# Kernel tuning notes

Measured on AMD Instinct MI355X. Metric: run time of the kernel, lower is better.

Reference implementation:

```python
import jax, jax.numpy as jnp
import numpy as np

N_NODES = 10000
N_EDGES = 160000
C = 128          # hidden_channels
H = 8            # heads
G = 16           # groups
L_LAYERS = 5
NUM_FEAT = 14
DIM_OUT = 16
CH = C // H      # channels per head (16)


def setup_inputs() -> dict:
    key = jax.random.key(0)
    ks = jax.random.split(key, 12)
    inp = {
        "x": jax.random.normal(ks[0], (N_NODES, NUM_FEAT), dtype=jnp.float32),
        "edge_index": jax.random.randint(ks[1], (2, N_EDGES), 0, N_NODES, dtype=jnp.int64),
        "lin1_w": jax.random.normal(ks[2], (NUM_FEAT, C), dtype=jnp.float32) * 0.1,
        "lin1_b": jax.random.normal(ks[3], (C,), dtype=jnp.float32) * 0.1,
        "Wq": jax.random.normal(ks[4], (L_LAYERS, G, C // G, C // G), dtype=jnp.float32) * 0.1,
        "bq": jax.random.normal(ks[5], (L_LAYERS, C), dtype=jnp.float32) * 0.1,
        "Wk": jax.random.normal(ks[6], (L_LAYERS, G, C // G, C // G), dtype=jnp.float32) * 0.1,
        "bk": jax.random.normal(ks[7], (L_LAYERS, C), dtype=jnp.float32) * 0.1,
        "Wv": jax.random.normal(ks[8], (L_LAYERS, G, C // G, C // G), dtype=jnp.float32) * 0.1,
        "bv": jax.random.normal(ks[9], (L_LAYERS, C), dtype=jnp.float32) * 0.1,
        "lin2_w": jax.random.normal(ks[10], (C, DIM_OUT), dtype=jnp.float32) * 0.1,
        "lin2_b": jax.random.normal(ks[11], (DIM_OUT,), dtype=jnp.float32) * 0.1,
    }
    return inp


def _grouped_linear(z, W, b):
    # z: [..., C]; W: [G, C/G, C/G]; b: [C]  (PyG grouped Linear)
    lead = z.shape[:-1]
    zg = z.reshape(lead + (G, C // G))
    out = jnp.einsum('...gi,gio->...go', zg, W)
    return out.reshape(lead + (C,)) + b


def _dna_forward(x, edge_index, lin1_w, lin1_b, Wq, bq, Wk, bk, Wv, bv, lin2_w, lin2_b):
    n = x.shape[0]
    # gcn_norm with self-loops (edge_weight = 1)
    loops = jnp.arange(n, dtype=edge_index.dtype)
    row = jnp.concatenate([edge_index[0], loops])  # sources (x_j)
    col = jnp.concatenate([edge_index[1], loops])  # targets (x_i, aggregation)
    ew = jnp.ones(row.shape[0], dtype=x.dtype)
    deg = jax.ops.segment_sum(ew, col, num_segments=n)
    dis = jax.lax.rsqrt(deg)  # deg >= 1 due to self-loops
    norm = dis[row] * dis[col]  # [Et]

    h = jax.nn.relu(x @ lin1_w + lin1_b)  # [N, C]
    x_all = h[:, None, :]                  # [N, 1, C]

    scale = 1.0 / np.sqrt(CH).astype(np.float32)
    for l in range(L_LAYERS):
        q = _grouped_linear(x_all[col, -1], Wq[l], bq[l])   # [Et, C]
        k = _grouped_linear(x_all[row], Wk[l], bk[l])       # [Et, L, C]
        v = _grouped_linear(x_all[row], Wv[l], bv[l])       # [Et, L, C]
        Et, Lh = k.shape[0], k.shape[1]
        qh = q.reshape(Et, H, CH)
        kh = k.reshape(Et, Lh, H, CH)
        vh = v.reshape(Et, Lh, H, CH)
        score = jnp.einsum('ehc,elhc->ehl', qh, kh) * scale
        attn = jax.nn.softmax(score, axis=-1)
        out = jnp.einsum('ehl,elhc->ehc', attn, vh).reshape(Et, C)
        msg = norm[:, None] * out
        agg = jax.ops.segment_sum(msg, col, num_segments=n)  # [N, C]
        xl = jax.nn.relu(agg)
        x_all = jnp.concatenate([x_all, xl[:, None, :]], axis=1)

    return x_all[:, -1] @ lin2_w + lin2_b  # [N, dim]


def reference(x, edge_index, lin1_w, lin1_b, Wq, bq, Wk, bk, Wv, bv, lin2_w, lin2_b):
    return _dna_forward(x, edge_index, lin1_w, lin1_b, Wq, bq, Wk, bk, Wv, bv,
                        lin2_w, lin2_b)
```

## Files before the change

kernel.cpp:

```cpp
#include <hip/hip_runtime.h>

#define N_NODES 10000
#define N_EDGESN 160000
#define E_TOT   (N_EDGESN + N_NODES)
#define C 128
#define H 8
#define G 16
#define LLAYERS 5
#define NUM_FEAT 14
#define DIM_OUT 16
#define CH 16
#define CG 8
#define X16STRIDE (6*C)

typedef _Float16 half8 __attribute__((ext_vector_type(8)));
typedef _Float16 half2v __attribute__((ext_vector_type(2)));

__global__ __launch_bounds__(256) void k_lin1(const float* __restrict__ x,
                                              const float* __restrict__ w,
                                              const float* __restrict__ b,
                                              _Float16* __restrict__ x16,
                                              int* __restrict__ counts) {
    __shared__ float sw[NUM_FEAT * C];
    __shared__ float sb[C];
    int tid = threadIdx.x;
    int gid = blockIdx.x * 256 + tid;
    if (gid < N_NODES) counts[gid] = 0;
    for (int i = tid; i < NUM_FEAT * C; i += 256) sw[i] = w[i];
    if (tid < C) sb[tid] = b[tid];
    __syncthreads();
    int node = blockIdx.x * 2 + tid / C;
    int c = tid & (C - 1);
    if (node >= N_NODES) return;
    const float* xr = x + node * NUM_FEAT;
    float acc = sb[c];
#pragma unroll
    for (int f = 0; f < NUM_FEAT; f++) acc += xr[f] * sw[f * C + c];
    acc = fmaxf(acc, 0.0f);
    x16[(size_t)node * X16STRIDE + c] = (_Float16)acc;
}

__global__ void k_count(const int* __restrict__ col, int* __restrict__ counts) {
    int e = blockIdx.x * blockDim.x + threadIdx.x;
    if (e < N_EDGESN) atomicAdd(&counts[col[e]], 1);
}

__global__ __launch_bounds__(1024) void k_scan(const int* __restrict__ counts,
                                               int* __restrict__ offs, int* __restrict__ cursor,
                                               float* __restrict__ dis,
                                               int* __restrict__ bucket_cur) {
    __shared__ int part[1024];
    __shared__ int hist[256];
    const int CHK = (N_NODES + 1023) / 1024;
    int t = threadIdx.x;
    if (t < 256) hist[t] = 0;
    __syncthreads();
    int base = t * CHK;
    int loc[CHK];
    int sum = 0;
#pragma unroll
    for (int i = 0; i < CHK; i++) {
        int idx = base + i;
        int v = (idx < N_NODES) ? (counts[idx] + 1) : 0;
        loc[i] = sum;
        sum += v;
        if (idx < N_NODES) atomicAdd(&hist[min(v, 255)], 1);
    }
    part[t] = sum;
    __syncthreads();
    for (int off = 1; off < 1024; off <<= 1) {
        int v = (t >= off) ? part[t - off] : 0;
        __syncthreads();
        part[t] += v;
        __syncthreads();
    }
    int prev = (t > 0) ? part[t - 1] : 0;
#pragma unroll
    for (int i = 0; i < CHK; i++) {
        int idx = base + i;
        if (idx < N_NODES) {
            int o = prev + loc[i];
            offs[idx] = o;
            cursor[idx] = o;
            dis[idx] = rsqrtf((float)(counts[idx] + 1));
        }
    }
    if (t == 1023) offs[N_NODES] = part[1023];
    __syncthreads();
    if (t == 0) {
        int acc = 0;
        for (int d2 = 255; d2 >= 0; d2--) { int h = hist[d2]; hist[d2] = acc; acc += h; }
    }
    __syncthreads();
    if (t < 256) bucket_cur[t] = hist[t];
}

__global__ void k_scatter(const int* __restrict__ row, const int* __restrict__ col,
                          const float* __restrict__ dis, const int* __restrict__ counts,
                          int* __restrict__ cursor, int2* __restrict__ csr,
                          int* __restrict__ bucket_cur, int* __restrict__ perm) {
    int e = blockIdx.x * blockDim.x + threadIdx.x;
    if (e < N_NODES) {
        int deg = min(counts[e] + 1, 255);
        int pos = atomicAdd(&bucket_cur[deg], 1);
        perm[pos] = e;
    }
    if (e >= E_TOT) return;
    int r = (e < N_EDGESN) ? row[e] : (e - N_EDGESN);
    int c = (e < N_EDGESN) ? col[e] : (e - N_EDGESN);
    int pos = atomicAdd(&cursor[c], 1);
    int2 pay;
    pay.x = r;
    pay.y = __float_as_int(dis[r]);
    csr[pos] = pay;
}

template <int NL>
__global__ __launch_bounds__(256) void k_attn_fly(const int* __restrict__ offs,
                                                  const int2* __restrict__ csr,
                                                  const float* __restrict__ dis,
                                                  const int* __restrict__ perm,
                                                  const float* __restrict__ Wq, const float* __restrict__ bq,
                                                  const float* __restrict__ Wk, const float* __restrict__ bk,
                                                  const float* __restrict__ Wv, const float* __restrict__ bv,
                                                  _Float16* __restrict__ x16) {
    const int l = NL - 1;
    int w = threadIdx.x >> 6;
    int lane = threadIdx.x & 63;
    int d = perm[blockIdx.x * 4 + w];
    int g = lane >> 2;
    int j4 = lane & 3;
    int c0 = 2 * lane;
    int o0 = 2 * j4;

    float y8[8];
    float z = 0.f;
    if constexpr (NL > 1) {
        half8 hq = *(const half8*)(x16 + (size_t)d * X16STRIDE + l * C + 8 * g);
        float xdv[8];
#pragma unroll
        for (int i = 0; i < 8; i++) xdv[i] = (float)hq[i];
        const float* bqg = bq + l * C + 8 * g;
        float4 qa = *(const float4*)bqg;
        float4 qb = *(const float4*)(bqg + 4);
        const float* wq = Wq + l * (G * CG * CG) + g * (CG * CG);
#pragma unroll
        for (int i = 0; i < 8; i++) {
            float4 ra = *(const float4*)(wq + i * CG);
            float4 rb = *(const float4*)(wq + i * CG + 4);
            qa.x += xdv[i] * ra.x; qa.y += xdv[i] * ra.y;
            qa.z += xdv[i] * ra.z; qa.w += xdv[i] * ra.w;
            qb.x += xdv[i] * rb.x; qb.y += xdv[i] * rb.y;
            qb.z += xdv[i] * rb.z; qb.w += xdv[i] * rb.w;
        }
        const float* wk = Wk + l * (G * CG * CG) + g * (CG * CG);
#pragma unroll
        for (int j = 0; j < 8; j++) {
            float4 ra = *(const float4*)(wk + j * CG);
            float4 rb = *(const float4*)(wk + j * CG + 4);
            y8[j] = qa.x * ra.x + qa.y * ra.y + qa.z * ra.z + qa.w * ra.w
                  + qb.x * rb.x + qb.y * rb.y + qb.z * rb.z + qb.w * rb.w;
        }
        const float* bkg = bk + l * C + 8 * g;
        float4 ba = *(const float4*)bkg;
        float4 bb = *(const float4*)(bkg + 4);
        z = qa.x * ba.x + qa.y * ba.y + qa.z * ba.z + qa.w * ba.w
          + qb.x * bb.x + qb.y * bb.y + qb.z * bb.z + qb.w * bb.w;
    }

    const float disd = dis[d];
    const int p0 = offs[d], p1 = offs[d + 1];
    const float scale = 0.25f;
    float xacc[8] = {0.f, 0.f, 0.f, 0.f, 0.f, 0.f, 0.f, 0.f};
    float nsum = 0.f;

    if constexpr (NL == 1) {
        for (int p = p0 + j4; p < p1; p += 4) {
            int2 pay = csr[p];
            float nrm = disd * __int_as_float(pay.y);
            half8 hv = *(const half8*)(x16 + (size_t)pay.x * X16STRIDE + 8 * g);
#pragma unroll
            for (int i = 0; i < 8; i++) xacc[i] += nrm * (float)hv[i];
            nsum += nrm;
        }
    } else {
        auto consume = [&](int2 pay, const half8 (&buf)[NL]) {
            float nrm = disd * __int_as_float(pay.y);
            float xv[NL][8];
            float sc[NL];
#pragma unroll
            for (int t = 0; t < NL; t++) {
#pragma unroll
                for (int i = 0; i < 8; i++) xv[t][i] = (float)buf[t][i];
                float part = z;
#pragma unroll
                for (int i = 0; i < 8; i++) part += xv[t][i] * y8[i];
                part += __shfl_xor(part, 4);
                sc[t] = part * scale;
            }
            float mx = sc[0];
#pragma unroll
            for (int t = 1; t < NL; t++) mx = fmaxf(mx, sc[t]);
            float s = 0.f;
            float ex[8] = {0.f, 0.f, 0.f, 0.f, 0.f, 0.f, 0.f, 0.f};
#pragma unroll
            for (int t = 0; t < NL; t++) {
                float e = __expf(sc[t] - mx);
                s += e;
#pragma unroll
                for (int i = 0; i < 8; i++) ex[i] += e * xv[t][i];
            }
            float inv = nrm * __builtin_amdgcn_rcpf(s);
#pragma unroll
            for (int i = 0; i < 8; i++) xacc[i] += inv * ex[i];
            nsum += nrm;
        };

        int p = p0 + j4;
        if (p < p1) {
            int2 payA = csr[p];
            half8 bufA[NL];
            {
                const _Float16* xs = x16 + (size_t)payA.x * X16STRIDE + 8 * g;
#pragma unroll
                for (int t = 0; t < NL; t++) bufA[t] = *(const half8*)(xs + t * C);
            }
            int pn = p + 4;
            int2 payB = csr[(pn < p1) ? pn : p];
            for (; pn < p1; pn += 4) {
                half8 bufB[NL];
                const _Float16* xs = x16 + (size_t)payB.x * X16STRIDE + 8 * g;
#pragma unroll
                for (int t = 0; t < NL; t++) bufB[t] = *(const half8*)(xs + t * C);
                int pc = pn + 4;
                int2 payC = csr[(pc < p1) ? pc : p0];
                consume(payA, bufA);
                payA = payB;
                payB = payC;
#pragma unroll
                for (int t = 0; t < NL; t++) bufA[t] = bufB[t];
            }
            consume(payA, bufA);
        }
    }

#pragma unroll
    for (int i = 0; i < 8; i++) {
        xacc[i] += __shfl_xor(xacc[i], 1);
        xacc[i] += __shfl_xor(xacc[i], 2);
    }
    nsum += __shfl_xor(nsum, 1);
    nsum += __shfl_xor(nsum, 2);

    const float* wv = Wv + l * (G * CG * CG) + g * (CG * CG);
    float a0 = bv[l * C + c0] * nsum;
    float a1 = bv[l * C + c0 + 1] * nsum;
#pragma unroll
    for (int i = 0; i < 8; i++) {
        a0 += xacc[i] * wv[i * CG + o0];
        a1 += xacc[i] * wv[i * CG + o0 + 1];
    }
    a0 = fmaxf(a0, 0.f);
    a1 = fmaxf(a1, 0.f);
    half2v ho;
    ho[0] = (_Float16)a0;
    ho[1] = (_Float16)a1;
    *(half2v*)(x16 + (size_t)d * X16STRIDE + (l + 1) * C + c0) = ho;
}

__global__ __launch_bounds__(256) void k_lin2(const _Float16* __restrict__ x16,
                                              const float* __restrict__ w,
                                              const float* __restrict__ b,
                                              float* __restrict__ out) {
    __shared__ float sw[C * DIM_OUT];
    __shared__ float sb[DIM_OUT];
    __shared__ float sx[16][C];
    int tid = threadIdx.x;
    for (int i = tid; i < C * DIM_OUT; i += 256) sw[i] = w[i];
    if (tid < DIM_OUT) sb[tid] = b[tid];
    int node0 = blockIdx.x * 16;
    {
        int nn = node0 + (tid >> 4);
        int co = (tid & 15) * 8;
        if (nn < N_NODES) {
            half8 hv = *(const half8*)(x16 + (size_t)nn * X16STRIDE + 5 * C + co);
#pragma unroll
            for (int i = 0; i < 8; i++) sx[tid >> 4][co + i] = (float)hv[i];
        } else {
#pragma unroll
            for (int i = 0; i < 8; i++) sx[tid >> 4][co + i] = 0.f;
        }
    }
    __syncthreads();
    int node = node0 + tid / DIM_OUT;
    int o = tid & (DIM_OUT - 1);
    if (node >= N_NODES) return;
    float acc = sb[o];
    const float* xr = sx[tid / DIM_OUT];
#pragma unroll 8
    for (int c = 0; c < C; c++) acc += xr[c] * sw[c * DIM_OUT + o];
    out[node * DIM_OUT + o] = acc;
}

extern "C" void kernel_launch(void* const* d_in, const int* in_sizes, int n_in,
                              void* d_out, int out_size, void* d_ws, size_t ws_size,
                              hipStream_t stream) {
    const float* x      = (const float*)d_in[0];
    const int*   edge   = (const int*)d_in[1];
    const int*   row    = edge;
    const int*   col    = edge + N_EDGESN;
    const float* lin1_w = (const float*)d_in[2];
    const float* lin1_b = (const float*)d_in[3];
    const float* Wq     = (const float*)d_in[4];
    const float* bq     = (const float*)d_in[5];
    const float* Wk     = (const float*)d_in[6];
    const float* bk     = (const float*)d_in[7];
    const float* Wv     = (const float*)d_in[8];
    const float* bv     = (const float*)d_in[9];
    const float* lin2_w = (const float*)d_in[10];
    const float* lin2_b = (const float*)d_in[11];
    float* outp = (float*)d_out;

    _Float16* x16   = (_Float16*)d_ws;
    int2*     csr   = (int2*)(x16 + (size_t)N_NODES * X16STRIDE);
    float*    dis   = (float*)(csr + E_TOT);
    int*   counts = (int*)(dis + N_NODES);
    int*   offs   = counts + N_NODES;
    int*   cursor = offs + N_NODES + 1;
    int*   bucket_cur = cursor + N_NODES;
    int*   perm   = bucket_cur + 256;

    k_lin1<<<N_NODES / 2, 256, 0, stream>>>(x, lin1_w, lin1_b, x16, counts);
    k_count<<<(N_EDGESN + 255) / 256, 256, 0, stream>>>(col, counts);
    k_scan<<<1, 1024, 0, stream>>>(counts, offs, cursor, dis, bucket_cur);
    k_scatter<<<(E_TOT + 255) / 256, 256, 0, stream>>>(row, col, dis, counts, cursor, csr, bucket_cur, perm);

    const int ablocks = N_NODES / 4;
    for (int l = 0; l < LLAYERS; l++) {
        switch (l) {
            case 0: k_attn_fly<1><<<ablocks, 256, 0, stream>>>(offs, csr, dis, perm, Wq, bq, Wk, bk, Wv, bv, x16); break;
            case 1: k_attn_fly<2><<<ablocks, 256, 0, stream>>>(offs, csr, dis, perm, Wq, bq, Wk, bk, Wv, bv, x16); break;
            case 2: k_attn_fly<3><<<ablocks, 256, 0, stream>>>(offs, csr, dis, perm, Wq, bq, Wk, bk, Wv, bv, x16); break;
            case 3: k_attn_fly<4><<<ablocks, 256, 0, stream>>>(offs, csr, dis, perm, Wq, bq, Wk, bk, Wv, bv, x16); break;
            case 4: k_attn_fly<5><<<ablocks, 256, 0, stream>>>(offs, csr, dis, perm, Wq, bq, Wk, bk, Wv, bv, x16); break;
        }
    }
    k_lin2<<<(N_NODES + 15) / 16, 256, 0, stream>>>(x16, lin2_w, lin2_b, outp);
}
```

Measured before the change: 242.2 us.

## Split each destination node's edge list across two wavefronts with LDS reduction

Each destination node is now processed by two wavefronts instead of one. Each wavefront strides over the incoming edges by 8, and the partial accumulators are combined through shared memory before the Wv projection and output write. The goal is more parallelism per node, shorter per-wave edge loops and better latency hiding on high-degree nodes. In exchange it doubles the block count, repeats the per-node q/k setup in both waves, and adds a __syncthreads plus LDS traffic.

```diff
diff --git a/kernel.cpp b/kernel.cpp
--- a/kernel.cpp
+++ b/kernel.cpp
@@ -14,7 +14,6 @@
 #define X16STRIDE (6*C)
 
 typedef _Float16 half8 __attribute__((ext_vector_type(8)));
-typedef _Float16 half2v __attribute__((ext_vector_type(2)));
 
 __global__ __launch_bounds__(256) void k_lin1(const float* __restrict__ x,
                                               const float* __restrict__ w,
@@ -125,13 +124,15 @@
                                                   const float* __restrict__ Wv, const float* __restrict__ bv,
                                                   _Float16* __restrict__ x16) {
     const int l = NL - 1;
+    __shared__ float red[4][C];
+    __shared__ float redn[4];
     int w = threadIdx.x >> 6;
     int lane = threadIdx.x & 63;
-    int d = perm[blockIdx.x * 4 + w];
+    int nsel = w >> 1;
+    int w2 = w & 1;
+    int d = perm[blockIdx.x * 2 + nsel];
     int g = lane >> 2;
     int j4 = lane & 3;
-    int c0 = 2 * lane;
-    int o0 = 2 * j4;
 
     float y8[8];
     float z = 0.f;
@@ -173,9 +174,10 @@
     const float scale = 0.25f;
     float xacc[8] = {0.f, 0.f, 0.f, 0.f, 0.f, 0.f, 0.f, 0.f};
     float nsum = 0.f;
+    const int s0 = w2 * 4 + j4;
 
     if constexpr (NL == 1) {
-        for (int p = p0 + j4; p < p1; p += 4) {
+        for (int p = p0 + s0; p < p1; p += 8) {
             int2 pay = csr[p];
             float nrm = disd * __int_as_float(pay.y);
             half8 hv = *(const half8*)(x16 + (size_t)pay.x * X16STRIDE + 8 * g);
@@ -216,7 +218,7 @@
             nsum += nrm;
         };
 
-        int p = p0 + j4;
+        int p = p0 + s0;
         if (p < p1) {
             int2 payA = csr[p];
             half8 bufA[NL];
@@ -225,14 +227,14 @@
 #pragma unroll
                 for (int t = 0; t < NL; t++) bufA[t] = *(const half8*)(xs + t * C);
             }
-            int pn = p + 4;
+            int pn = p + 8;
             int2 payB = csr[(pn < p1) ? pn : p];
-            for (; pn < p1; pn += 4) {
+            for (; pn < p1; pn += 8) {
                 half8 bufB[NL];
                 const _Float16* xs = x16 + (size_t)payB.x * X16STRIDE + 8 * g;
 #pragma unroll
                 for (int t = 0; t < NL; t++) bufB[t] = *(const half8*)(xs + t * C);
-                int pc = pn + 4;
+                int pc = pn + 8;
                 int2 payC = csr[(pc < p1) ? pc : p0];
                 consume(payA, bufA);
                 payA = payB;
@@ -252,20 +254,27 @@
     nsum += __shfl_xor(nsum, 1);
     nsum += __shfl_xor(nsum, 2);
 
-    const float* wv = Wv + l * (G * CG * CG) + g * (CG * CG);
-    float a0 = bv[l * C + c0] * nsum;
-    float a1 = bv[l * C + c0 + 1] * nsum;
-#pragma unroll
-    for (int i = 0; i < 8; i++) {
-        a0 += xacc[i] * wv[i * CG + o0];
-        a1 += xacc[i] * wv[i * CG + o0 + 1];
-    }
-    a0 = fmaxf(a0, 0.f);
-    a1 = fmaxf(a1, 0.f);
-    half2v ho;
-    ho[0] = (_Float16)a0;
-    ho[1] = (_Float16)a1;
-    *(half2v*)(x16 + (size_t)d * X16STRIDE + (l + 1) * C + c0) = ho;
+    if (j4 == 0) {
+#pragma unroll
+        for (int i = 0; i < 8; i++) red[w][8 * g + i] = xacc[i];
+    }
+    if (lane == 0) redn[w] = nsum;
+    __syncthreads();
+
+    {
+        int ns2 = threadIdx.x >> 7;
+        int c = threadIdx.x & 127;
+        int dd = perm[blockIdx.x * 2 + ns2];
+        float ns = redn[2 * ns2] + redn[2 * ns2 + 1];
+        int gg = c >> 3, oo = c & 7;
+        const float* wv = Wv + l * (G * CG * CG) + gg * (CG * CG);
+        float acc = bv[l * C + c] * ns;
+#pragma unroll
+        for (int i = 0; i < 8; i++)
+            acc += (red[2 * ns2][8 * gg + i] + red[2 * ns2 + 1][8 * gg + i]) * wv[i * CG + oo];
+        acc = fmaxf(acc, 0.f);
+        x16[(size_t)dd * X16STRIDE + (l + 1) * C + c] = (_Float16)acc;
+    }
 }
 
 __global__ __launch_bounds__(256) void k_lin2(const _Float16* __restrict__ x16,
@@ -335,7 +344,7 @@
     k_scan<<<1, 1024, 0, stream>>>(counts, offs, cursor, dis, bucket_cur);
     k_scatter<<<(E_TOT + 255) / 256, 256, 0, stream>>>(row, col, dis, counts, cursor, csr, bucket_cur, perm);
 
-    const int ablocks = N_NODES / 4;
+    const int ablocks = N_NODES / 2;
     for (int l = 0; l < LLAYERS; l++) {
         switch (l) {
             case 0: k_attn_fly<1><<<ablocks, 256, 0, stream>>>(offs, csr, dis, perm, Wq, bq, Wk, bk, Wv, bv, x16); break;
```

Measured after the change: 281.6 us. 1.16x slower.
